# Kernel optimization log

Hardware: AMD Instinct MI355X
Metric: run time of the kernel (lower is better)

Reference implementation:

```python
import jax, jax.numpy as jnp
import numpy as np

HIDDEN = 1024
N_HEAD = 16
D_HEAD = HIDDEN // N_HEAD  # 64


def setup_inputs() -> dict:
    key = jax.random.key(0)
    ks = jax.random.split(key, 7)
    B, S = 2, 2048
    sd = 1.0 / np.sqrt(HIDDEN)
    return {
        "query": jax.random.normal(ks[0], (B, S, HIDDEN), jnp.float32),
        "key": jax.random.normal(ks[1], (B, S, HIDDEN), jnp.float32),
        "value": jax.random.normal(ks[2], (B, S, HIDDEN), jnp.float32),
        # per-head projection weights, stacked over heads: [H, hidden, d_head]
        "Wq": jax.random.normal(ks[3], (N_HEAD, HIDDEN, D_HEAD), jnp.float32) * sd,
        "Wk": jax.random.normal(ks[4], (N_HEAD, HIDDEN, D_HEAD), jnp.float32) * sd,
        "Wv": jax.random.normal(ks[5], (N_HEAD, HIDDEN, D_HEAD), jnp.float32) * sd,
        # output projection [hidden, hidden] (applied as x @ Wo)
        "Wo": jax.random.normal(ks[6], (HIDDEN, HIDDEN), jnp.float32) * sd,
    }


def reference(query, key, value, Wq, Wk, Wv, Wo):
    # Per-head projections (vectorized over heads instead of Python loop)
    q = jnp.einsum("bsd,hdk->bhsk", query, Wq)   # [B,H,S,Dh]
    k = jnp.einsum("btd,hdk->bhtk", key, Wk)     # [B,H,T,Dh]
    v = jnp.einsum("btd,hdk->bhtk", value, Wv)   # [B,H,T,Dh]

    scale = jnp.sqrt(jnp.asarray(D_HEAD, q.dtype))
    scores = jnp.einsum("bhsk,bhtk->bhst", q, k) / scale  # [B,H,S,T]
    attn = jax.nn.softmax(scores, axis=-1)                 # attention_score
    # dropout is identity in eval / p=0
    wv = jnp.einsum("bhst,bhtk->bhsk", attn, v)            # [B,H,S,Dh]

    B, H, S, Dh = wv.shape
    concat = wv.transpose(0, 2, 1, 3).reshape(B, S, H * Dh)  # head concat
    out = concat @ Wo                                         # o_w projection
    return out, attn
```

## Files before the change

### kernel.cpp

```cpp
#include <hip/hip_runtime.h>
#include <hip/hip_bf16.h>


#define SEQ 2048
#define NH 16

typedef short short8 __attribute__((ext_vector_type(8)));
typedef short short4s __attribute__((ext_vector_type(4)));
typedef float f32x4 __attribute__((ext_vector_type(4)));

static __device__ __forceinline__ short f2bf(float f) {
  __hip_bfloat16 h = __float2bfloat16(f);
  return *reinterpret_cast<const short*>(&h);
}

static __device__ __forceinline__ f32x4 mfma16(short8 a, short8 b, f32x4 c) {
  return __builtin_amdgcn_mfma_f32_16x16x32_bf16(a, b, c, 0, 0, 0);
}

__global__ __launch_bounds__(256) void wt_kernel(
    const float* __restrict__ Wq, const float* __restrict__ Wk,
    const float* __restrict__ Wv, const float* __restrict__ Wo,
    short* __restrict__ wtq, short* __restrict__ wtk,
    short* __restrict__ wtv, short* __restrict__ wot) {
  int bid = blockIdx.x;
  const float* src;
  short* dst;
  int sstride;
  if (bid < 768) {
    int mat = bid >> 8;
    int rem = bid & 255;
    int h = rem >> 4, kt = rem & 15;
    const float* W = (mat == 0) ? Wq : ((mat == 1) ? Wk : Wv);
    short* wt = (mat == 0) ? wtq : ((mat == 1) ? wtk : wtv);
    src = W + h * 65536 + kt * 64 * 64;
    sstride = 64;
    dst = wt + h * 65536 + kt * 64;
  } else {
    int idx = bid - 768;
    int nt = idx >> 4, kt = idx & 15;
    src = Wo + kt * 64 * 1024 + nt * 64;
    sstride = 1024;
    dst = wot + nt * 64 * 1024 + kt * 64;
  }
  int t = threadIdx.x;
  int c0 = t >> 2, ch = t & 3;
  short vals[16];
#pragma unroll
  for (int e = 0; e < 16; ++e)
    vals[e] = f2bf(src[(ch * 16 + e) * sstride + c0]);
  short8 lo, hi;
#pragma unroll
  for (int e = 0; e < 8; ++e) { lo[e] = vals[e]; hi[e] = vals[8 + e]; }
  *reinterpret_cast<short8*>(dst + c0 * 1024 + ch * 16) = lo;
  *reinterpret_cast<short8*>(dst + c0 * 1024 + ch * 16 + 8) = hi;
}

template <bool AF32, bool OUTF32>
static __device__ __forceinline__ void gemm_body(
    const void* __restrict__ Aptr, const short* __restrict__ Bt,
    void* __restrict__ outp, float scale, int m0, int n0) {
  __shared__ short As[64][72];
  __shared__ short Bs[128][72];
  int tid = threadIdx.x, lane = tid & 63, wid = tid >> 6;
  int wm = wid >> 1, wn = wid & 1;
  int lg = lane >> 4, ll = lane & 15;

  f32x4 zero = {0.f, 0.f, 0.f, 0.f};
  f32x4 acc[2][4];
#pragma unroll
  for (int mf = 0; mf < 2; ++mf)
#pragma unroll
    for (int nf = 0; nf < 4; ++nf) acc[mf][nf] = zero;

  for (int k0 = 0; k0 < 1024; k0 += 64) {
    if (k0) __syncthreads();
    if (AF32) {
      const float* A = (const float*)Aptr;
      int r = tid >> 2, sub = tid & 3;
      const float* ap = A + (size_t)(m0 + r) * 1024 + k0;
#pragma unroll
      for (int rep = 0; rep < 4; ++rep) {
        int c = rep * 16 + sub * 4;
        f32x4 v = *reinterpret_cast<const f32x4*>(ap + c);
        short4s o;
#pragma unroll
        for (int j = 0; j < 4; ++j) o[j] = f2bf(v[j]);
        *reinterpret_cast<short4s*>(&As[r][c]) = o;
      }
    } else {
      const short* A = (const short*)Aptr;
      int r = tid >> 2, sub = tid & 3;
      const short* ap = A + (size_t)(m0 + r) * 1024 + k0 + sub * 16;
      *reinterpret_cast<short8*>(&As[r][sub * 16]) =
          *reinterpret_cast<const short8*>(ap);
      *reinterpret_cast<short8*>(&As[r][sub * 16 + 8]) =
          *reinterpret_cast<const short8*>(ap + 8);
    }
    {
      int nr = tid >> 1, hp = tid & 1;
      const short* bp = Bt + (size_t)(n0 + nr) * 1024 + k0;
#pragma unroll
      for (int rep = 0; rep < 2; ++rep) {
#pragma unroll
        for (int h8 = 0; h8 < 2; ++h8) {
          int c = rep * 32 + hp * 16 + h8 * 8;
          *reinterpret_cast<short8*>(&Bs[nr][c]) =
              *reinterpret_cast<const short8*>(bp + c);
        }
      }
    }
    __syncthreads();

    short8 af[2][2], bf[4][2];
#pragma unroll
    for (int mf = 0; mf < 2; ++mf)
#pragma unroll
      for (int kc = 0; kc < 2; ++kc)
        af[mf][kc] = *reinterpret_cast<const short8*>(
            &As[wm * 32 + mf * 16 + ll][kc * 32 + lg * 8]);
#pragma unroll
    for (int nf = 0; nf < 4; ++nf)
#pragma unroll
      for (int kc = 0; kc < 2; ++kc)
        bf[nf][kc] = *reinterpret_cast<const short8*>(
            &Bs[wn * 64 + nf * 16 + ll][kc * 32 + lg * 8]);
#pragma unroll
    for (int mf = 0; mf < 2; ++mf)
#pragma unroll
      for (int nf = 0; nf < 4; ++nf)
#pragma unroll
        for (int kc = 0; kc < 2; ++kc)
          acc[mf][nf] = mfma16(af[mf][kc], bf[nf][kc], acc[mf][nf]);
  }

  if (OUTF32) {
    float* out = (float*)outp;
#pragma unroll
    for (int mf = 0; mf < 2; ++mf)
#pragma unroll
      for (int nf = 0; nf < 4; ++nf) {
        int ncol = n0 + wn * 64 + nf * 16 + ll;
        int mbase = m0 + wm * 32 + mf * 16 + lg * 4;
#pragma unroll
        for (int j = 0; j < 4; ++j)
          out[(size_t)(mbase + j) * 1024 + ncol] = acc[mf][nf][j];
      }
  } else {
    short* out = (short*)outp;
#pragma unroll
    for (int mf = 0; mf < 2; ++mf)
#pragma unroll
      for (int nf = 0; nf < 4; ++nf) {
        int ncol = n0 + wn * 64 + nf * 16 + ll;
        int h = ncol >> 6, dh = ncol & 63;
        int mbase = m0 + wm * 32 + mf * 16 + lg * 4;
#pragma unroll
        for (int j = 0; j < 4; ++j) {
          int m = mbase + j;
          int b = m >> 11, s = m & 2047;
          out[(size_t)((b * NH + h) * SEQ + s) * 64 + dh] =
              f2bf(acc[mf][nf][j] * scale);
        }
      }
  }
}

__global__ __launch_bounds__(256) void gemm_qkv_kernel(
    const float* __restrict__ q, const float* __restrict__ k,
    const float* __restrict__ v, const short* __restrict__ wtq,
    const short* __restrict__ wtk, const short* __restrict__ wtv,
    short* __restrict__ qp, short* __restrict__ kp, short* __restrict__ vp) {
  int z = blockIdx.z;
  const float* A = (z == 0) ? q : ((z == 1) ? k : v);
  const short* Bt = (z == 0) ? wtq : ((z == 1) ? wtk : wtv);
  short* out = (z == 0) ? qp : ((z == 1) ? kp : vp);
  float scale = (z == 0) ? 0.125f : 1.0f;
  gemm_body<true, false>(A, Bt, out, scale, blockIdx.x * 64, blockIdx.y * 128);
}

__global__ __launch_bounds__(256) void gemm_out_kernel(
    const short* __restrict__ wv, const short* __restrict__ wot,
    float* __restrict__ outp) {
  gemm_body<false, true>(wv, wot, outp, 1.0f, blockIdx.x * 64,
                         blockIdx.y * 128);
}

__global__ __launch_bounds__(256) void attn_kernel(
    const short* __restrict__ qp, const short* __restrict__ kp,
    const short* __restrict__ vp, float* __restrict__ attn,
    short* __restrict__ wv) {
  __shared__ short Ks[64][72];
  __shared__ short Vt[64][72];
  __shared__ short Ps[4][16][72];
  int tid = threadIdx.x, lane = tid & 63, wid = tid >> 6;
  int lg = lane >> 4, ll = lane & 15;
  int bh = blockIdx.y;
  int q0 = blockIdx.x * 64;

  const short* qb = qp + (size_t)(bh * SEQ + q0 + wid * 16 + ll) * 64;
  short8 qf[2];
  qf[0] = *reinterpret_cast<const short8*>(qb + lg * 8);
  qf[1] = *reinterpret_cast<const short8*>(qb + 32 + lg * 8);

  const short* kb = kp + (size_t)bh * SEQ * 64;
  const short* vb = vp + (size_t)bh * SEQ * 64;
  f32x4 zero = {0.f, 0.f, 0.f, 0.f};

  float lsum[4] = {0.f, 0.f, 0.f, 0.f};
  for (int t0 = 0; t0 < SEQ; t0 += 64) {
    if (t0) __syncthreads();
    {
      int tr = tid >> 2, cp = tid & 3;
      const short* sp = kb + (size_t)(t0 + tr) * 64 + cp * 16;
      *reinterpret_cast<short8*>(&Ks[tr][cp * 16]) =
          *reinterpret_cast<const short8*>(sp);
      *reinterpret_cast<short8*>(&Ks[tr][cp * 16 + 8]) =
          *reinterpret_cast<const short8*>(sp + 8);
    }
    __syncthreads();
    f32x4 sacc[4] = {zero, zero, zero, zero};
#pragma unroll
    for (int tf = 0; tf < 4; ++tf) {
      short8 kf0 = *reinterpret_cast<const short8*>(&Ks[tf * 16 + ll][lg * 8]);
      short8 kf1 =
          *reinterpret_cast<const short8*>(&Ks[tf * 16 + ll][32 + lg * 8]);
      sacc[tf] = mfma16(qf[0], kf0, sacc[tf]);
      sacc[tf] = mfma16(qf[1], kf1, sacc[tf]);
    }
#pragma unroll
    for (int tf = 0; tf < 4; ++tf)
#pragma unroll
      for (int j = 0; j < 4; ++j) lsum[j] += __expf(sacc[tf][j]);
  }
#pragma unroll
  for (int j = 0; j < 4; ++j) {
    lsum[j] += __shfl_xor(lsum[j], 1);
    lsum[j] += __shfl_xor(lsum[j], 2);
    lsum[j] += __shfl_xor(lsum[j], 4);
    lsum[j] += __shfl_xor(lsum[j], 8);
  }
  float linv[4];
#pragma unroll
  for (int j = 0; j < 4; ++j) linv[j] = 1.0f / lsum[j];

  f32x4 oacc[4] = {zero, zero, zero, zero};
  for (int t0 = 0; t0 < SEQ; t0 += 64) {
    __syncthreads();
    {
      int tr = tid >> 2, cp = tid & 3;
      const short* sp = kb + (size_t)(t0 + tr) * 64 + cp * 16;
      *reinterpret_cast<short8*>(&Ks[tr][cp * 16]) =
          *reinterpret_cast<const short8*>(sp);
      *reinterpret_cast<short8*>(&Ks[tr][cp * 16 + 8]) =
          *reinterpret_cast<const short8*>(sp + 8);
    }
    {
      int t = tid & 63, dq = tid >> 6;
      const short* sp = vb + (size_t)(t0 + t) * 64 + dq * 16;
      short8 v0 = *reinterpret_cast<const short8*>(sp);
      short8 v1 = *reinterpret_cast<const short8*>(sp + 8);
#pragma unroll
      for (int e = 0; e < 8; ++e) Vt[dq * 16 + e][t] = v0[e];
#pragma unroll
      for (int e = 0; e < 8; ++e) Vt[dq * 16 + 8 + e][t] = v1[e];
    }
    __syncthreads();
    f32x4 sacc[4] = {zero, zero, zero, zero};
#pragma unroll
    for (int tf = 0; tf < 4; ++tf) {
      short8 kf0 = *reinterpret_cast<const short8*>(&Ks[tf * 16 + ll][lg * 8]);
      short8 kf1 =
          *reinterpret_cast<const short8*>(&Ks[tf * 16 + ll][32 + lg * 8]);
      sacc[tf] = mfma16(qf[0], kf0, sacc[tf]);
      sacc[tf] = mfma16(qf[1], kf1, sacc[tf]);
    }
    float p[4][4];
#pragma unroll
    for (int tf = 0; tf < 4; ++tf)
#pragma unroll
      for (int j = 0; j < 4; ++j) p[tf][j] = __expf(sacc[tf][j]) * linv[j];
#pragma unroll
    for (int j = 0; j < 4; ++j) {
      int qr = wid * 16 + lg * 4 + j;
      float* arow = attn + (size_t)(bh * SEQ + q0 + qr) * SEQ + t0 + ll;
#pragma unroll
      for (int tf = 0; tf < 4; ++tf) arow[tf * 16] = p[tf][j];
    }
#pragma unroll
    for (int tf = 0; tf < 4; ++tf)
#pragma unroll
      for (int j = 0; j < 4; ++j)
        Ps[wid][lg * 4 + j][tf * 16 + ll] = f2bf(p[tf][j]);
    short8 pa0 = *reinterpret_cast<const short8*>(&Ps[wid][ll][lg * 8]);
    short8 pa1 = *reinterpret_cast<const short8*>(&Ps[wid][ll][32 + lg * 8]);
#pragma unroll
    for (int df = 0; df < 4; ++df) {
      short8 vf0 = *reinterpret_cast<const short8*>(&Vt[df * 16 + ll][lg * 8]);
      short8 vf1 =
          *reinterpret_cast<const short8*>(&Vt[df * 16 + ll][32 + lg * 8]);
      oacc[df] = mfma16(pa0, vf0, oacc[df]);
      oacc[df] = mfma16(pa1, vf1, oacc[df]);
    }
  }
  int b = bh >> 4, h = bh & 15;
#pragma unroll
  for (int df = 0; df < 4; ++df)
#pragma unroll
    for (int j = 0; j < 4; ++j) {
      int s = q0 + wid * 16 + lg * 4 + j;
      wv[(size_t)(b * SEQ + s) * 1024 + h * 64 + df * 16 + ll] =
          f2bf(oacc[df][j]);
    }
}

extern "C" void kernel_launch(void* const* d_in, const int* in_sizes, int n_in,
                              void* d_out, int out_size, void* d_ws,
                              size_t ws_size, hipStream_t stream) {
  const float* query = (const float*)d_in[0];
  const float* key = (const float*)d_in[1];
  const float* value = (const float*)d_in[2];
  const float* Wq = (const float*)d_in[3];
  const float* Wk = (const float*)d_in[4];
  const float* Wv = (const float*)d_in[5];
  const float* Wo = (const float*)d_in[6];

  float* outp = (float*)d_out;
  float* attnp = outp + 4194304;

  short* ws = (short*)d_ws;
  short* qp = ws;
  short* kpp = ws + 4194304;
  short* vpp = ws + 8388608;
  short* wvp = ws + 12582912;
  short* wtq = ws + 16777216;
  short* wtk = wtq + 1048576;
  short* wtv = wtk + 1048576;
  short* wot = wtv + 1048576;

  wt_kernel<<<dim3(1024), 256, 0, stream>>>(Wq, Wk, Wv, Wo, wtq, wtk, wtv,
                                            wot);
  gemm_qkv_kernel<<<dim3(64, 8, 3), 256, 0, stream>>>(
      query, key, value, wtq, wtk, wtv, qp, kpp, vpp);
  attn_kernel<<<dim3(32, 32), 256, 0, stream>>>(qp, kpp, vpp, attnp, wvp);
  gemm_out_kernel<<<dim3(64, 8), 256, 0, stream>>>(wvp, wot, outp);
}
```

Before: 758.4 us.

## Restructure attention: transposed swizzled V, direct LDS loads, larger query tiles

The QKV GEMM now writes K with an XOR-swizzled column layout and V pre-transposed (with its own swizzle), so the attention kernel can load K and V tiles straight into LDS via global_load_lds without padding or a per-element transpose. Each wave handles 32 query rows instead of 16, which halves how often K/V tiles are loaded per query. The grid is flattened to 1D and mapped so that heads are grouped per XCD for L2 locality. Attention probabilities are written with nontemporal stores. This adds coupling between the GEMM epilogue layout and the attention reader, and uses more registers per wave.

```diff
diff --git a/kernel.cpp b/kernel.cpp
--- a/kernel.cpp
+++ b/kernel.cpp
@@ -16,6 +16,12 @@
 
 static __device__ __forceinline__ f32x4 mfma16(short8 a, short8 b, f32x4 c) {
   return __builtin_amdgcn_mfma_f32_16x16x32_bf16(a, b, c, 0, 0, 0);
+}
+
+static __device__ __forceinline__ void gload16(const void* g, void* l) {
+  __builtin_amdgcn_global_load_lds(
+      (const __attribute__((address_space(1))) void*)g,
+      (__attribute__((address_space(3))) void*)l, 16, 0, 0);
 }
 
 __global__ __launch_bounds__(256) void wt_kernel(
@@ -59,7 +65,7 @@
 template <bool AF32, bool OUTF32>
 static __device__ __forceinline__ void gemm_body(
     const void* __restrict__ Aptr, const short* __restrict__ Bt,
-    void* __restrict__ outp, float scale, int m0, int n0) {
+    void* __restrict__ outp, float scale, int m0, int n0, int mode) {
   __shared__ short As[64][72];
   __shared__ short Bs[128][72];
   int tid = threadIdx.x, lane = tid & 63, wid = tid >> 6;
@@ -101,14 +107,13 @@
       int nr = tid >> 1, hp = tid & 1;
       const short* bp = Bt + (size_t)(n0 + nr) * 1024 + k0;
 #pragma unroll
-      for (int rep = 0; rep < 2; ++rep) {
+      for (int rep = 0; rep < 2; ++rep)
 #pragma unroll
         for (int h8 = 0; h8 < 2; ++h8) {
           int c = rep * 32 + hp * 16 + h8 * 8;
           *reinterpret_cast<short8*>(&Bs[nr][c]) =
               *reinterpret_cast<const short8*>(bp + c);
         }
-      }
     }
     __syncthreads();
 
@@ -155,12 +160,22 @@
         int ncol = n0 + wn * 64 + nf * 16 + ll;
         int h = ncol >> 6, dh = ncol & 63;
         int mbase = m0 + wm * 32 + mf * 16 + lg * 4;
-#pragma unroll
-        for (int j = 0; j < 4; ++j) {
-          int m = mbase + j;
-          int b = m >> 11, s = m & 2047;
-          out[(size_t)((b * NH + h) * SEQ + s) * 64 + dh] =
-              f2bf(acc[mf][nf][j] * scale);
+        int b = mbase >> 11, s0 = mbase & 2047;
+        if (mode == 3) {
+          short4s o4;
+#pragma unroll
+          for (int j = 0; j < 4; ++j) o4[j] = f2bf(acc[mf][nf][j]);
+          size_t idx = ((size_t)((b * NH + h) * 64 + dh)) * SEQ +
+                       (s0 ^ ((dh & 7) << 3));
+          *reinterpret_cast<short4s*>(out + idx) = o4;
+        } else {
+#pragma unroll
+          for (int j = 0; j < 4; ++j) {
+            int s = s0 + j;
+            int dh2 = (mode == 2) ? (dh ^ ((s & 7) << 3)) : dh;
+            out[(size_t)((b * NH + h) * SEQ + s) * 64 + dh2] =
+                f2bf(acc[mf][nf][j] * scale);
+          }
         }
       }
   }
@@ -176,142 +191,169 @@
   const short* Bt = (z == 0) ? wtq : ((z == 1) ? wtk : wtv);
   short* out = (z == 0) ? qp : ((z == 1) ? kp : vp);
   float scale = (z == 0) ? 0.125f : 1.0f;
-  gemm_body<true, false>(A, Bt, out, scale, blockIdx.x * 64, blockIdx.y * 128);
+  gemm_body<true, false>(A, Bt, out, scale, blockIdx.x * 64, blockIdx.y * 128,
+                         z + 1);
 }
 
 __global__ __launch_bounds__(256) void gemm_out_kernel(
     const short* __restrict__ wv, const short* __restrict__ wot,
     float* __restrict__ outp) {
   gemm_body<false, true>(wv, wot, outp, 1.0f, blockIdx.x * 64,
-                         blockIdx.y * 128);
+                         blockIdx.y * 128, 0);
 }
 
 __global__ __launch_bounds__(256) void attn_kernel(
     const short* __restrict__ qp, const short* __restrict__ kp,
-    const short* __restrict__ vp, float* __restrict__ attn,
+    const short* __restrict__ vpt, float* __restrict__ attn,
     short* __restrict__ wv) {
-  __shared__ short Ks[64][72];
-  __shared__ short Vt[64][72];
-  __shared__ short Ps[4][16][72];
+  __shared__ short Ks[64][64];
+  __shared__ short Vs[64][64];
+  __shared__ short Ps[4][32][72];
   int tid = threadIdx.x, lane = tid & 63, wid = tid >> 6;
   int lg = lane >> 4, ll = lane & 15;
-  int bh = blockIdx.y;
-  int q0 = blockIdx.x * 64;
-
-  const short* qb = qp + (size_t)(bh * SEQ + q0 + wid * 16 + ll) * 64;
-  short8 qf[2];
-  qf[0] = *reinterpret_cast<const short8*>(qb + lg * 8);
-  qf[1] = *reinterpret_cast<const short8*>(qb + 32 + lg * 8);
-
-  const short* kb = kp + (size_t)bh * SEQ * 64;
-  const short* vb = vp + (size_t)bh * SEQ * 64;
+  int bid = blockIdx.x;
+  int xcd = bid & 7, li = bid >> 3;
+  int bh = xcd * 4 + (li >> 4);
+  int q0 = (li & 15) * 128;
+  int wq0 = q0 + wid * 32;
+
+  short8 qf[2][2];
+#pragma unroll
+  for (int mf = 0; mf < 2; ++mf) {
+    const short* qr =
+        qp + (size_t)(bh * SEQ + wq0 + mf * 16 + ll) * 64;
+    qf[mf][0] = *reinterpret_cast<const short8*>(qr + lg * 8);
+    qf[mf][1] = *reinterpret_cast<const short8*>(qr + 32 + lg * 8);
+  }
+  const short* kb = kp + (size_t)(bh * SEQ) * 64;
+  const short* vtb = vpt + (size_t)bh * 64 * SEQ;
+  int sc = (ll & 7) << 3;
   f32x4 zero = {0.f, 0.f, 0.f, 0.f};
 
-  float lsum[4] = {0.f, 0.f, 0.f, 0.f};
+  float lsum[2][4] = {{0.f, 0.f, 0.f, 0.f}, {0.f, 0.f, 0.f, 0.f}};
   for (int t0 = 0; t0 < SEQ; t0 += 64) {
-    if (t0) __syncthreads();
+    __syncthreads();
     {
-      int tr = tid >> 2, cp = tid & 3;
-      const short* sp = kb + (size_t)(t0 + tr) * 64 + cp * 16;
-      *reinterpret_cast<short8*>(&Ks[tr][cp * 16]) =
-          *reinterpret_cast<const short8*>(sp);
-      *reinterpret_cast<short8*>(&Ks[tr][cp * 16 + 8]) =
-          *reinterpret_cast<const short8*>(sp + 8);
-    }
-    __syncthreads();
-    f32x4 sacc[4] = {zero, zero, zero, zero};
-#pragma unroll
-    for (int tf = 0; tf < 4; ++tf) {
-      short8 kf0 = *reinterpret_cast<const short8*>(&Ks[tf * 16 + ll][lg * 8]);
-      short8 kf1 =
-          *reinterpret_cast<const short8*>(&Ks[tf * 16 + ll][32 + lg * 8]);
-      sacc[tf] = mfma16(qf[0], kf0, sacc[tf]);
-      sacc[tf] = mfma16(qf[1], kf1, sacc[tf]);
-    }
-#pragma unroll
-    for (int tf = 0; tf < 4; ++tf)
-#pragma unroll
-      for (int j = 0; j < 4; ++j) lsum[j] += __expf(sacc[tf][j]);
-  }
-#pragma unroll
-  for (int j = 0; j < 4; ++j) {
-    lsum[j] += __shfl_xor(lsum[j], 1);
-    lsum[j] += __shfl_xor(lsum[j], 2);
-    lsum[j] += __shfl_xor(lsum[j], 4);
-    lsum[j] += __shfl_xor(lsum[j], 8);
-  }
-  float linv[4];
-#pragma unroll
-  for (int j = 0; j < 4; ++j) linv[j] = 1.0f / lsum[j];
-
-  f32x4 oacc[4] = {zero, zero, zero, zero};
+      const short* kt = kb + (size_t)t0 * 64;
+#pragma unroll
+      for (int it = 0; it < 2; ++it) {
+        int o = it * 2048 + wid * 512;
+        gload16(kt + o + lane * 8, &Ks[0][0] + o);
+      }
+    }
+    __syncthreads();
+#pragma unroll
+    for (int mf = 0; mf < 2; ++mf) {
+      f32x4 sacc[4] = {zero, zero, zero, zero};
+#pragma unroll
+      for (int tf = 0; tf < 4; ++tf) {
+        const short* krow = &Ks[tf * 16 + ll][0];
+        short8 kf0 = *reinterpret_cast<const short8*>(krow + ((lg * 8) ^ sc));
+        short8 kf1 =
+            *reinterpret_cast<const short8*>(krow + ((32 + lg * 8) ^ sc));
+        sacc[tf] = mfma16(qf[mf][0], kf0, sacc[tf]);
+        sacc[tf] = mfma16(qf[mf][1], kf1, sacc[tf]);
+      }
+#pragma unroll
+      for (int tf = 0; tf < 4; ++tf)
+#pragma unroll
+        for (int j = 0; j < 4; ++j) lsum[mf][j] += __expf(sacc[tf][j]);
+    }
+  }
+#pragma unroll
+  for (int mf = 0; mf < 2; ++mf)
+#pragma unroll
+    for (int j = 0; j < 4; ++j) {
+      float v = lsum[mf][j];
+      v += __shfl_xor(v, 1);
+      v += __shfl_xor(v, 2);
+      v += __shfl_xor(v, 4);
+      v += __shfl_xor(v, 8);
+      lsum[mf][j] = 1.0f / v;
+    }
+
+  f32x4 oacc[2][4];
+#pragma unroll
+  for (int mf = 0; mf < 2; ++mf)
+#pragma unroll
+    for (int df = 0; df < 4; ++df) oacc[mf][df] = zero;
+
   for (int t0 = 0; t0 < SEQ; t0 += 64) {
     __syncthreads();
     {
-      int tr = tid >> 2, cp = tid & 3;
-      const short* sp = kb + (size_t)(t0 + tr) * 64 + cp * 16;
-      *reinterpret_cast<short8*>(&Ks[tr][cp * 16]) =
-          *reinterpret_cast<const short8*>(sp);
-      *reinterpret_cast<short8*>(&Ks[tr][cp * 16 + 8]) =
-          *reinterpret_cast<const short8*>(sp + 8);
-    }
-    {
-      int t = tid & 63, dq = tid >> 6;
-      const short* sp = vb + (size_t)(t0 + t) * 64 + dq * 16;
-      short8 v0 = *reinterpret_cast<const short8*>(sp);
-      short8 v1 = *reinterpret_cast<const short8*>(sp + 8);
-#pragma unroll
-      for (int e = 0; e < 8; ++e) Vt[dq * 16 + e][t] = v0[e];
-#pragma unroll
-      for (int e = 0; e < 8; ++e) Vt[dq * 16 + 8 + e][t] = v1[e];
-    }
-    __syncthreads();
-    f32x4 sacc[4] = {zero, zero, zero, zero};
-#pragma unroll
-    for (int tf = 0; tf < 4; ++tf) {
-      short8 kf0 = *reinterpret_cast<const short8*>(&Ks[tf * 16 + ll][lg * 8]);
-      short8 kf1 =
-          *reinterpret_cast<const short8*>(&Ks[tf * 16 + ll][32 + lg * 8]);
-      sacc[tf] = mfma16(qf[0], kf0, sacc[tf]);
-      sacc[tf] = mfma16(qf[1], kf1, sacc[tf]);
-    }
-    float p[4][4];
-#pragma unroll
-    for (int tf = 0; tf < 4; ++tf)
-#pragma unroll
-      for (int j = 0; j < 4; ++j) p[tf][j] = __expf(sacc[tf][j]) * linv[j];
-#pragma unroll
-    for (int j = 0; j < 4; ++j) {
-      int qr = wid * 16 + lg * 4 + j;
-      float* arow = attn + (size_t)(bh * SEQ + q0 + qr) * SEQ + t0 + ll;
-#pragma unroll
-      for (int tf = 0; tf < 4; ++tf) arow[tf * 16] = p[tf][j];
-    }
-#pragma unroll
-    for (int tf = 0; tf < 4; ++tf)
-#pragma unroll
-      for (int j = 0; j < 4; ++j)
-        Ps[wid][lg * 4 + j][tf * 16 + ll] = f2bf(p[tf][j]);
-    short8 pa0 = *reinterpret_cast<const short8*>(&Ps[wid][ll][lg * 8]);
-    short8 pa1 = *reinterpret_cast<const short8*>(&Ps[wid][ll][32 + lg * 8]);
-#pragma unroll
-    for (int df = 0; df < 4; ++df) {
-      short8 vf0 = *reinterpret_cast<const short8*>(&Vt[df * 16 + ll][lg * 8]);
-      short8 vf1 =
-          *reinterpret_cast<const short8*>(&Vt[df * 16 + ll][32 + lg * 8]);
-      oacc[df] = mfma16(pa0, vf0, oacc[df]);
-      oacc[df] = mfma16(pa1, vf1, oacc[df]);
+      const short* kt = kb + (size_t)t0 * 64;
+#pragma unroll
+      for (int it = 0; it < 2; ++it) {
+        int o = it * 2048 + wid * 512;
+        gload16(kt + o + lane * 8, &Ks[0][0] + o);
+      }
+#pragma unroll
+      for (int it = 0; it < 2; ++it) {
+        int o = it * 2048 + wid * 512;
+        int ol = o + lane * 8;
+        int r = ol >> 6, c = ol & 63;
+        gload16(vtb + (size_t)r * SEQ + t0 + c, &Vs[0][0] + o);
+      }
+    }
+    __syncthreads();
+#pragma unroll
+    for (int mf = 0; mf < 2; ++mf) {
+      f32x4 sacc[4] = {zero, zero, zero, zero};
+#pragma unroll
+      for (int tf = 0; tf < 4; ++tf) {
+        const short* krow = &Ks[tf * 16 + ll][0];
+        short8 kf0 = *reinterpret_cast<const short8*>(krow + ((lg * 8) ^ sc));
+        short8 kf1 =
+            *reinterpret_cast<const short8*>(krow + ((32 + lg * 8) ^ sc));
+        sacc[tf] = mfma16(qf[mf][0], kf0, sacc[tf]);
+        sacc[tf] = mfma16(qf[mf][1], kf1, sacc[tf]);
+      }
+      float p[4][4];
+#pragma unroll
+      for (int tf = 0; tf < 4; ++tf)
+#pragma unroll
+        for (int j = 0; j < 4; ++j)
+          p[tf][j] = __expf(sacc[tf][j]) * lsum[mf][j];
+#pragma unroll
+      for (int j = 0; j < 4; ++j) {
+        float* arow =
+            attn + (size_t)(bh * SEQ + wq0 + mf * 16 + lg * 4 + j) * SEQ +
+            t0 + ll;
+#pragma unroll
+        for (int tf = 0; tf < 4; ++tf)
+          __builtin_nontemporal_store(p[tf][j], arow + tf * 16);
+      }
+#pragma unroll
+      for (int tf = 0; tf < 4; ++tf)
+#pragma unroll
+        for (int j = 0; j < 4; ++j)
+          Ps[wid][mf * 16 + lg * 4 + j][tf * 16 + ll] = f2bf(p[tf][j]);
+      short8 pa0 =
+          *reinterpret_cast<const short8*>(&Ps[wid][mf * 16 + ll][lg * 8]);
+      short8 pa1 = *reinterpret_cast<const short8*>(
+          &Ps[wid][mf * 16 + ll][32 + lg * 8]);
+#pragma unroll
+      for (int df = 0; df < 4; ++df) {
+        const short* vrow = &Vs[df * 16 + ll][0];
+        short8 vf0 = *reinterpret_cast<const short8*>(vrow + ((lg * 8) ^ sc));
+        short8 vf1 =
+            *reinterpret_cast<const short8*>(vrow + ((32 + lg * 8) ^ sc));
+        oacc[mf][df] = mfma16(pa0, vf0, oacc[mf][df]);
+        oacc[mf][df] = mfma16(pa1, vf1, oacc[mf][df]);
+      }
     }
   }
   int b = bh >> 4, h = bh & 15;
 #pragma unroll
-  for (int df = 0; df < 4; ++df)
-#pragma unroll
-    for (int j = 0; j < 4; ++j) {
-      int s = q0 + wid * 16 + lg * 4 + j;
-      wv[(size_t)(b * SEQ + s) * 1024 + h * 64 + df * 16 + ll] =
-          f2bf(oacc[df][j]);
-    }
+  for (int mf = 0; mf < 2; ++mf)
+#pragma unroll
+    for (int df = 0; df < 4; ++df)
+#pragma unroll
+      for (int j = 0; j < 4; ++j) {
+        int s = wq0 + mf * 16 + lg * 4 + j;
+        wv[(size_t)(b * SEQ + s) * 1024 + h * 64 + df * 16 + ll] =
+            f2bf(oacc[mf][df][j]);
+      }
 }
 
 extern "C" void kernel_launch(void* const* d_in, const int* in_sizes, int n_in,
@@ -331,7 +373,7 @@
   short* ws = (short*)d_ws;
   short* qp = ws;
   short* kpp = ws + 4194304;
-  short* vpp = ws + 8388608;
+  short* vpt = ws + 8388608;
   short* wvp = ws + 12582912;
   short* wtq = ws + 16777216;
   short* wtk = wtq + 1048576;
@@ -341,7 +383,7 @@
   wt_kernel<<<dim3(1024), 256, 0, stream>>>(Wq, Wk, Wv, Wo, wtq, wtk, wtv,
                                             wot);
   gemm_qkv_kernel<<<dim3(64, 8, 3), 256, 0, stream>>>(
-      query, key, value, wtq, wtk, wtv, qp, kpp, vpp);
-  attn_kernel<<<dim3(32, 32), 256, 0, stream>>>(qp, kpp, vpp, attnp, wvp);
+      query, key, value, wtq, wtk, wtv, qp, kpp, vpt);
+  attn_kernel<<<dim3(512), 256, 0, stream>>>(qp, kpp, vpt, attnp, wvp);
   gemm_out_kernel<<<dim3(64, 8), 256, 0, stream>>>(wvp, wot, outp);
 }
```

Result: no change. 745.2 us (-1.7%).
